# Performance work log

Measured on AMD Instinct MI355X. Metric: run time of the kernel, lower is better.

Reference implementation:

```python
import jax, jax.numpy as jnp
import numpy as np

N_NODES = 50000


def _gat_layer(h, e_feat, Ww, Wb, aw, ab, src, dst):
    # h: [N,1,din], e_feat: [E,1,edim]
    hs = h[src]                                   # [E,1,din] gather src
    hd = h[dst]                                   # [E,1,din] gather dst
    # edge attention logit: relu(attn_fc(cat(src,dst)))
    e = jax.nn.relu(jnp.concatenate([hs, hd], axis=-1) @ aw.T + ab)  # [E,1,1]
    # segment softmax over incoming edges of each dst node
    emax = jax.ops.segment_max(e, dst, num_segments=N_NODES)          # [N,1,1]
    ex = jnp.exp(e - emax[dst])
    denom = jax.ops.segment_sum(ex, dst, num_segments=N_NODES)        # [N,1,1]
    alpha = ex / denom[dst]                                           # [E,1,1]
    # weighted scatter-sum of edge messages (m = edge features)
    z = jax.ops.segment_sum(alpha * e_feat, dst, num_segments=N_NODES)  # [N,1,edim]
    # node update: relu(W_apply(cat(h, z)))
    return jax.nn.relu(jnp.concatenate([h, z], axis=-1) @ Ww.T + Wb)    # [N,1,dout]


def setup_inputs() -> dict:
    key = jax.random.key(0)
    ks = jax.random.split(key, 12)
    N, E, D = N_NODES, 640000, 128
    s = 0.05  # weight scale for numerical sanity
    return {
        "nfeats": jax.random.normal(ks[0], (N, 1, D), jnp.float32),
        "efeats": jax.random.normal(ks[1], (E, 1, D), jnp.float32),
        "W_apply_w0": jax.random.normal(ks[2], (D, 2 * D), jnp.float32) * s,
        "W_apply_b0": jax.random.normal(ks[3], (D,), jnp.float32) * s,
        "attn_w0": jax.random.normal(ks[4], (1, 2 * D), jnp.float32) * s,
        "attn_b0": jax.random.normal(ks[5], (1,), jnp.float32) * s,
        "W_apply_w1": jax.random.normal(ks[6], (D, 2 * D), jnp.float32) * s,
        "W_apply_b1": jax.random.normal(ks[7], (D,), jnp.float32) * s,
        "attn_w1": jax.random.normal(ks[8], (1, 2 * D), jnp.float32) * s,
        "attn_b1": jax.random.normal(ks[9], (1,), jnp.float32) * s,
        "src": jax.random.randint(ks[10], (E,), 0, N, jnp.int32),
        "dst": jax.random.randint(ks[11], (E,), 0, N, jnp.int32),
    }


def reference(nfeats, efeats, W_apply_w0, W_apply_b0, attn_w0, attn_b0,
              W_apply_w1, W_apply_b1, attn_w1, attn_b1, src, dst):
    h = _gat_layer(nfeats, efeats, W_apply_w0, W_apply_b0, attn_w0, attn_b0, src, dst)
    # dropout is identity in eval mode
    h = _gat_layer(h, efeats, W_apply_w1, W_apply_b1, attn_w1, attn_b1, src, dst)
    return h.sum(axis=1)  # [N, dout]
```

## Files before the change

### kernel.cpp

```cpp
#include <hip/hip_runtime.h>


__global__ void hist_k(const int* __restrict__ dst, int* __restrict__ counts, int E){
  int e = blockIdx.x*blockDim.x + threadIdx.x;
  if(e<E) atomicAdd(&counts[dst[e]], 1);
}

__global__ __launch_bounds__(1024) void scan1_k(const int* __restrict__ counts, int* __restrict__ excl,
                                                int* __restrict__ partials, int N){
  __shared__ int tmp[1024];
  int tid = threadIdx.x;
  int i = blockIdx.x*1024 + tid;
  int v = (i<N)? counts[i] : 0;
  tmp[tid] = v;
  __syncthreads();
  for(int off=1; off<1024; off<<=1){
    int t = (tid>=off)? tmp[tid-off] : 0;
    __syncthreads();
    tmp[tid] += t;
    __syncthreads();
  }
  if(i<N) excl[i] = tmp[tid] - v;
  if(tid==1023) partials[blockIdx.x] = tmp[tid];
}

__global__ void scan2_k(int* __restrict__ partials, int NB){
  __shared__ int tmp[64];
  int tid = threadIdx.x;
  int v = (tid<NB)? partials[tid] : 0;
  tmp[tid] = v;
  __syncthreads();
  for(int off=1; off<64; off<<=1){
    int t = (tid>=off)? tmp[tid-off] : 0;
    __syncthreads();
    tmp[tid] += t;
    __syncthreads();
  }
  if(tid<NB) partials[tid] = tmp[tid] - v;
}

__global__ __launch_bounds__(1024) void scan3_k(int* __restrict__ row_ptr, const int* __restrict__ partials,
                                                int* __restrict__ cursors, int N, int E){
  int i = blockIdx.x*1024 + threadIdx.x;
  if(i<N){
    int r = row_ptr[i] + partials[blockIdx.x];
    row_ptr[i] = r;
    cursors[i] = r;
  }
  if(i==0) row_ptr[N] = E;
}

__global__ void scatter_k(const int* __restrict__ src, const int* __restrict__ dst, int* __restrict__ cursors,
                          int2* __restrict__ edat, int E){
  int e = blockIdx.x*blockDim.x + threadIdx.x;
  if(e<E){
    int d = dst[e];
    int p = atomicAdd(&cursors[d], 1);
    edat[p] = make_int2(e, src[e]);
  }
}

__global__ void wt_k(const float* __restrict__ W, float* __restrict__ Wt){
  int idx = blockIdx.x*256 + threadIdx.x;
  int k = idx >> 7, o = idx & 127;
  Wt[idx] = W[o*256 + k];
}


__global__ void attn_k(const float* __restrict__ h, const float* __restrict__ aw, const float* __restrict__ ab,
                       float* __restrict__ a_src, float* __restrict__ a_dst, int N){
  int gid = blockIdx.x*blockDim.x + threadIdx.x;
  int n = gid >> 6, lane = gid & 63;
  if(n >= N) return;
  float2 hv = ((const float2*)(h + (size_t)n*128))[lane];
  float2 wa = ((const float2*)aw)[lane];
  float2 wb = ((const float2*)(aw+128))[lane];
  float s = hv.x*wa.x + hv.y*wa.y;
  float t = hv.x*wb.x + hv.y*wb.y;
  #pragma unroll
  for(int off=32; off>0; off>>=1){
    s += __shfl_xor(s, off, 64);
    t += __shfl_xor(t, off, 64);
  }
  if(lane==0){ a_src[n] = s; a_dst[n] = t + ab[0]; }
}

__global__ __launch_bounds__(256) void agg_k(const float* __restrict__ efeats,
    const float* __restrict__ a_src, const float* __restrict__ a_dst,
    const int* __restrict__ row_ptr, const int2* __restrict__ edat,
    float* __restrict__ z, int N){
  int gid = blockIdx.x*blockDim.x + threadIdx.x;
  int n = gid >> 6, lane = gid & 63;
  if(n >= N) return;
  int half = lane >> 5, l32 = lane & 31;
  int beg = row_ptr[n], end = row_ptr[n+1];
  int deg = end - beg;
  if(deg <= 0){
    if(half==0) ((float4*)z)[(size_t)n*32 + l32] = make_float4(0.f,0.f,0.f,0.f);
    return;
  }
  float adn = a_dst[n];

  int i = beg + lane;
  bool valid = i < end;
  int2 es = valid ? edat[i] : make_int2(0,0);
  int perm_reg = es.x;
  float e_reg = valid ? fmaxf(a_src[es.y] + adn, 0.f) : -1e30f;

  float m = e_reg;
  #pragma unroll
  for(int off=32; off>0; off>>=1) m = fmaxf(m, __shfl_xor(m, off, 64));
  for(int c = beg + 64; c < end; c += 64){
    int ii = c + lane;
    float ev = (ii < end) ? fmaxf(a_src[edat[ii].y] + adn, 0.f) : -1e30f;
    #pragma unroll
    for(int off=32; off>0; off>>=1) ev = fmaxf(ev, __shfl_xor(ev, off, 64));
    m = fmaxf(m, ev);
  }

  float ex_reg = valid ? __expf(e_reg - m) : 0.f;
  float s = ex_reg;
  #pragma unroll
  for(int off=32; off>0; off>>=1) s += __shfl_xor(s, off, 64);
  for(int c = beg + 64; c < end; c += 64){
    int ii = c + lane;
    float ev = (ii < end) ? __expf(fmaxf(a_src[edat[ii].y] + adn, 0.f) - m) : 0.f;
    #pragma unroll
    for(int off=32; off>0; off>>=1) ev += __shfl_xor(ev, off, 64);
    s += ev;
  }
  float inv = 1.f / s;

  const float4* ef4 = (const float4*)efeats;
  float4 acc = make_float4(0.f,0.f,0.f,0.f);
  int cnt = min(deg, 64);
  int j = 0;
  for(; j + 8 <= cnt; j += 8){
    float p0 = __shfl(ex_reg, j+half,   64); int r0 = __shfl(perm_reg, j+half,   64);
    float p1 = __shfl(ex_reg, j+2+half, 64); int r1 = __shfl(perm_reg, j+2+half, 64);
    float p2 = __shfl(ex_reg, j+4+half, 64); int r2 = __shfl(perm_reg, j+4+half, 64);
    float p3 = __shfl(ex_reg, j+6+half, 64); int r3 = __shfl(perm_reg, j+6+half, 64);
    float4 f0 = ef4[(size_t)r0*32 + l32];
    float4 f1 = ef4[(size_t)r1*32 + l32];
    float4 f2 = ef4[(size_t)r2*32 + l32];
    float4 f3 = ef4[(size_t)r3*32 + l32];
    acc.x += p0*f0.x; acc.y += p0*f0.y; acc.z += p0*f0.z; acc.w += p0*f0.w;
    acc.x += p1*f1.x; acc.y += p1*f1.y; acc.z += p1*f1.z; acc.w += p1*f1.w;
    acc.x += p2*f2.x; acc.y += p2*f2.y; acc.z += p2*f2.z; acc.w += p2*f2.w;
    acc.x += p3*f3.x; acc.y += p3*f3.y; acc.z += p3*f3.z; acc.w += p3*f3.w;
  }
  for(; j + 2 <= cnt; j += 2){
    float p = __shfl(ex_reg, j+half, 64); int r = __shfl(perm_reg, j+half, 64);
    float4 f = ef4[(size_t)r*32 + l32];
    acc.x += p*f.x; acc.y += p*f.y; acc.z += p*f.z; acc.w += p*f.w;
  }
  if(j < cnt){
    float p = __shfl(ex_reg, j, 64); int r = __shfl(perm_reg, j, 64);
    if(half==0){
      float4 f = ef4[(size_t)r*32 + l32];
      acc.x += p*f.x; acc.y += p*f.y; acc.z += p*f.z; acc.w += p*f.w;
    }
  }
  for(int c = beg + 64; c < end; c += 64){
    int ii = c + lane;
    bool v2 = ii < end;
    int2 es2 = v2 ? edat[ii] : make_int2(0,0);
    int pr = es2.x;
    float er = v2 ? __expf(fmaxf(a_src[es2.y] + adn, 0.f) - m) : 0.f;
    int cc = min(end - c, 64);
    int jj = 0;
    for(; jj + 2 <= cc; jj += 2){
      float p = __shfl(er, jj+half, 64); int r = __shfl(pr, jj+half, 64);
      float4 f = ef4[(size_t)r*32 + l32];
      acc.x += p*f.x; acc.y += p*f.y; acc.z += p*f.z; acc.w += p*f.w;
    }
    if(jj < cc){
      float p = __shfl(er, jj, 64); int r = __shfl(pr, jj, 64);
      if(half==0){
        float4 f = ef4[(size_t)r*32 + l32];
        acc.x += p*f.x; acc.y += p*f.y; acc.z += p*f.z; acc.w += p*f.w;
      }
    }
  }

  acc.x += __shfl_xor(acc.x, 32, 64);
  acc.y += __shfl_xor(acc.y, 32, 64);
  acc.z += __shfl_xor(acc.z, 32, 64);
  acc.w += __shfl_xor(acc.w, 32, 64);
  if(half==0){
    acc.x *= inv; acc.y *= inv; acc.z *= inv; acc.w *= inv;
    ((float4*)z)[(size_t)n*32 + l32] = acc;
  }
}

__global__ __launch_bounds__(256) void update_k(const float* __restrict__ h, const float* __restrict__ z,
                                                const float* __restrict__ Wt, const float* __restrict__ bias,
                                                float* __restrict__ out, int N){
  __shared__ float xsT[32][132];
  __shared__ float ws[32][132];
  int tid = threadIdx.x;
  int tx = tid & 15;
  int ty = tid >> 4;
  int n0 = blockIdx.x * 128;

  int sn  = tid >> 1;
  int skc = (tid & 1) * 16;
  int wkk = tid >> 3;
  int woc = (tid & 7) * 4;

  float4 xv4[4], wv4[4];
  {
    int node = n0 + sn;
    bool v = node < N;
    const float* sp = h + (size_t)node*128 + skc;
    #pragma unroll
    for(int jj=0;jj<4;jj++) xv4[jj] = v ? ((const float4*)sp)[jj] : make_float4(0.f,0.f,0.f,0.f);
    const float* wp = Wt + (size_t)wkk*128 + woc;
    #pragma unroll
    for(int jj=0;jj<4;jj++) wv4[jj] = *(const float4*)(wp + jj*32);
  }

  float acc[8][8];
  #pragma unroll
  for(int i=0;i<8;i++)
    #pragma unroll
    for(int j2=0;j2<8;j2++) acc[i][j2] = 0.f;

  for(int kb=0; kb<256; kb+=32){
    #pragma unroll
    for(int jj=0;jj<4;jj++){
      int kq = skc + jj*4;
      xsT[kq+0][sn] = xv4[jj].x;
      xsT[kq+1][sn] = xv4[jj].y;
      xsT[kq+2][sn] = xv4[jj].z;
      xsT[kq+3][sn] = xv4[jj].w;
      *(float4*)&ws[wkk][woc + jj*32] = wv4[jj];
    }
    __syncthreads();

    if(kb + 32 < 256){
      int kb2 = kb + 32;
      int node = n0 + sn;
      bool v = node < N;
      const float* sp = (kb2 < 128) ? h + (size_t)node*128 + kb2 + skc
                                    : z + (size_t)node*128 + (kb2-128) + skc;
      #pragma unroll
      for(int jj=0;jj<4;jj++) xv4[jj] = v ? ((const float4*)sp)[jj] : make_float4(0.f,0.f,0.f,0.f);
      const float* wp = Wt + (size_t)(kb2 + wkk)*128 + woc;
      #pragma unroll
      for(int jj=0;jj<4;jj++) wv4[jj] = *(const float4*)(wp + jj*32);
    }

    #pragma unroll 8
    for(int k=0;k<32;k++){
      float4 x0 = *(const float4*)&xsT[k][ty*4];
      float4 x1 = *(const float4*)&xsT[k][64 + ty*4];
      float4 w0 = *(const float4*)&ws[k][tx*4];
      float4 w1 = *(const float4*)&ws[k][64 + tx*4];
      float xv[8] = {x0.x,x0.y,x0.z,x0.w, x1.x,x1.y,x1.z,x1.w};
      float wv[8] = {w0.x,w0.y,w0.z,w0.w, w1.x,w1.y,w1.z,w1.w};
      #pragma unroll
      for(int i=0;i<8;i++)
        #pragma unroll
        for(int j2=0;j2<8;j2++)
          acc[i][j2] += xv[i]*wv[j2];
    }
    __syncthreads();
  }

  const float4* b4 = (const float4*)bias;
  float4 bb0 = b4[tx];
  float4 bb1 = b4[16 + tx];
  #pragma unroll
  for(int i=0;i<8;i++){
    int n = n0 + ((i<4) ? (ty*4 + i) : (64 + ty*4 + (i-4)));
    if(n >= N) continue;
    float4 r0, r1;
    r0.x = fmaxf(acc[i][0]+bb0.x, 0.f);
    r0.y = fmaxf(acc[i][1]+bb0.y, 0.f);
    r0.z = fmaxf(acc[i][2]+bb0.z, 0.f);
    r0.w = fmaxf(acc[i][3]+bb0.w, 0.f);
    r1.x = fmaxf(acc[i][4]+bb1.x, 0.f);
    r1.y = fmaxf(acc[i][5]+bb1.y, 0.f);
    r1.z = fmaxf(acc[i][6]+bb1.z, 0.f);
    r1.w = fmaxf(acc[i][7]+bb1.w, 0.f);
    *(float4*)(out + (size_t)n*128 + tx*4)      = r0;
    *(float4*)(out + (size_t)n*128 + 64 + tx*4) = r1;
  }
}


extern "C" void kernel_launch(void* const* d_in, const int* in_sizes, int n_in,
                              void* d_out, int out_size, void* d_ws, size_t ws_size,
                              hipStream_t stream){
  const float* nfeats = (const float*)d_in[0];
  const float* efeats = (const float*)d_in[1];
  const float* Ww0 = (const float*)d_in[2];
  const float* Wb0 = (const float*)d_in[3];
  const float* aw0 = (const float*)d_in[4];
  const float* ab0 = (const float*)d_in[5];
  const float* Ww1 = (const float*)d_in[6];
  const float* Wb1 = (const float*)d_in[7];
  const float* aw1 = (const float*)d_in[8];
  const float* ab1 = (const float*)d_in[9];
  const int* src = (const int*)d_in[10];
  const int* dst = (const int*)d_in[11];
  int E = in_sizes[10];
  int N = in_sizes[0] / 128;

  char* base = (char*)d_ws;
  size_t off = 0;
  auto take = [&](size_t bytes) -> char* {
    char* p = base + off;
    off = (off + bytes + 255) & ~(size_t)255;
    return p;
  };
  int*   counts  = (int*)take((size_t)N*4);
  int*   row_ptr = (int*)take((size_t)(N+1)*4);
  int*   cursors = (int*)take((size_t)N*4);
  int*   partials= (int*)take(256);
  int2*  edat    = (int2*)take((size_t)E*8);
  float* a_src   = (float*)take((size_t)N*4);
  float* a_dst   = (float*)take((size_t)N*4);
  float* zbuf    = (float*)take((size_t)N*128*4);
  float* h1      = (float*)take((size_t)N*128*4);
  float* Wt0     = (float*)take((size_t)256*128*4);
  float* Wt1     = (float*)take((size_t)256*128*4);

  int NB = (N + 1023)/1024;

  hipMemsetAsync(counts, 0, (size_t)N*4, stream);
  wt_k<<<128, 256, 0, stream>>>(Ww0, Wt0);
  wt_k<<<128, 256, 0, stream>>>(Ww1, Wt1);
  hist_k<<<(E+255)/256, 256, 0, stream>>>(dst, counts, E);
  scan1_k<<<NB, 1024, 0, stream>>>(counts, row_ptr, partials, N);
  scan2_k<<<1, 64, 0, stream>>>(partials, NB);
  scan3_k<<<NB, 1024, 0, stream>>>(row_ptr, partials, cursors, N, E);
  scatter_k<<<(E+255)/256, 256, 0, stream>>>(src, dst, cursors, edat, E);

  int agrid = (N + 3)/4;
  int ugrid = (N + 127)/128;
  attn_k<<<agrid, 256, 0, stream>>>(nfeats, aw0, ab0, a_src, a_dst, N);
  agg_k<<<agrid, 256, 0, stream>>>(efeats, a_src, a_dst, row_ptr, edat, zbuf, N);
  update_k<<<ugrid, 256, 0, stream>>>(nfeats, zbuf, Wt0, Wb0, h1, N);
  attn_k<<<agrid, 256, 0, stream>>>(h1, aw1, ab1, a_src, a_dst, N);
  agg_k<<<agrid, 256, 0, stream>>>(efeats, a_src, a_dst, row_ptr, edat, zbuf, N);
  update_k<<<ugrid, 256, 0, stream>>>(h1, zbuf, Wt1, Wb1, (float*)d_out, N);
}
```

Measured before the change: 773.8 us.

## Fuse CSR preprocessing kernels, single-block scan, and shrink update tile to 64 nodes

Merges the two weight transposes and the dst histogram into one grid-stride kernel. It replaces the three-kernel block scan with a single 1024-thread block that does a wave-shuffle scan with a running carry. It also fuses the edge scatter into the first attention-logit kernel. Separately, the node update GEMM now uses 64-node tiles with 128 threads, doubling the block count for better CU coverage. The goal is to cut kernel launches and serialization, at the cost of a serial single-block scan and less per-block reuse of the weight tiles.

```diff
diff --git a/kernel.cpp b/kernel.cpp
--- a/kernel.cpp
+++ b/kernel.cpp
@@ -1,71 +1,85 @@
 #include <hip/hip_runtime.h>
 
-
-__global__ void hist_k(const int* __restrict__ dst, int* __restrict__ counts, int E){
-  int e = blockIdx.x*blockDim.x + threadIdx.x;
-  if(e<E) atomicAdd(&counts[dst[e]], 1);
-}
-
-__global__ __launch_bounds__(1024) void scan1_k(const int* __restrict__ counts, int* __restrict__ excl,
-                                                int* __restrict__ partials, int N){
-  __shared__ int tmp[1024];
+__global__ void prep_k(const float* __restrict__ Ww0, const float* __restrict__ Ww1,
+                       float* __restrict__ Wt0, float* __restrict__ Wt1,
+                       const int* __restrict__ dst, int* __restrict__ counts, int E){
+  int gid = blockIdx.x*blockDim.x + threadIdx.x;
+  int gstride = gridDim.x*blockDim.x;
+  for(int idx = gid; idx < 2*32768; idx += gstride){
+    int w = idx >> 15, r = idx & 32767;
+    int k = r >> 7, o = r & 127;
+    float v = (w==0 ? Ww0 : Ww1)[o*256 + k];
+    (w==0 ? Wt0 : Wt1)[r] = v;
+  }
+  for(int e = gid; e < E; e += gstride) atomicAdd(&counts[dst[e]], 1);
+}
+
+__global__ __launch_bounds__(1024) void scan_k(const int* __restrict__ counts,
+                                               int* __restrict__ row_ptr, int* __restrict__ cursors,
+                                               int N, int E){
+  __shared__ int wsum[16];
+  __shared__ int carry;
   int tid = threadIdx.x;
-  int i = blockIdx.x*1024 + tid;
-  int v = (i<N)? counts[i] : 0;
-  tmp[tid] = v;
+  int lane = tid & 63, wv = tid >> 6;
+  if(tid==0) carry = 0;
   __syncthreads();
-  for(int off=1; off<1024; off<<=1){
-    int t = (tid>=off)? tmp[tid-off] : 0;
-    __syncthreads();
-    tmp[tid] += t;
-    __syncthreads();
-  }
-  if(i<N) excl[i] = tmp[tid] - v;
-  if(tid==1023) partials[blockIdx.x] = tmp[tid];
-}
-
-__global__ void scan2_k(int* __restrict__ partials, int NB){
-  __shared__ int tmp[64];
-  int tid = threadIdx.x;
-  int v = (tid<NB)? partials[tid] : 0;
-  tmp[tid] = v;
-  __syncthreads();
-  for(int off=1; off<64; off<<=1){
-    int t = (tid>=off)? tmp[tid-off] : 0;
-    __syncthreads();
-    tmp[tid] += t;
-    __syncthreads();
-  }
-  if(tid<NB) partials[tid] = tmp[tid] - v;
-}
-
-__global__ __launch_bounds__(1024) void scan3_k(int* __restrict__ row_ptr, const int* __restrict__ partials,
-                                                int* __restrict__ cursors, int N, int E){
-  int i = blockIdx.x*1024 + threadIdx.x;
-  if(i<N){
-    int r = row_ptr[i] + partials[blockIdx.x];
-    row_ptr[i] = r;
-    cursors[i] = r;
-  }
-  if(i==0) row_ptr[N] = E;
-}
-
-__global__ void scatter_k(const int* __restrict__ src, const int* __restrict__ dst, int* __restrict__ cursors,
-                          int2* __restrict__ edat, int E){
-  int e = blockIdx.x*blockDim.x + threadIdx.x;
-  if(e<E){
-    int d = dst[e];
+  for(int base = 0; base < N; base += 1024){
+    int i = base + tid;
+    int v = (i<N) ? counts[i] : 0;
+    int x = v;
+    #pragma unroll
+    for(int off=1; off<64; off<<=1){
+      int t = __shfl_up(x, off, 64);
+      if(lane >= off) x += t;
+    }
+    if(lane==63) wsum[wv] = x;
+    __syncthreads();
+    if(tid < 16){
+      int w = wsum[tid];
+      #pragma unroll
+      for(int off=1; off<16; off<<=1){
+        int t = __shfl_up(w, off, 64);
+        if(tid >= off) w += t;
+      }
+      wsum[tid] = w;
+    }
+    __syncthreads();
+    int prev = (wv==0) ? 0 : wsum[wv-1];
+    int ex = carry + prev + x - v;
+    if(i<N){ row_ptr[i] = ex; cursors[i] = ex; }
+    __syncthreads();
+    if(tid==0) carry += wsum[15];
+    __syncthreads();
+  }
+  if(tid==0) row_ptr[N] = E;
+}
+
+__global__ void scat_attn_k(const int* __restrict__ src, const int* __restrict__ dst,
+                            int* __restrict__ cursors, int2* __restrict__ edat, int E,
+                            const float* __restrict__ h, const float* __restrict__ aw,
+                            const float* __restrict__ ab,
+                            float* __restrict__ a_src, float* __restrict__ a_dst, int N){
+  int gid = blockIdx.x*blockDim.x + threadIdx.x;
+  if(gid < E){
+    int d = dst[gid];
     int p = atomicAdd(&cursors[d], 1);
-    edat[p] = make_int2(e, src[e]);
-  }
-}
-
-__global__ void wt_k(const float* __restrict__ W, float* __restrict__ Wt){
-  int idx = blockIdx.x*256 + threadIdx.x;
-  int k = idx >> 7, o = idx & 127;
-  Wt[idx] = W[o*256 + k];
-}
-
+    edat[p] = make_int2(gid, src[gid]);
+  }
+  int n = gid >> 6, lane = gid & 63;
+  if(n < N){
+    float2 hv = ((const float2*)(h + (size_t)n*128))[lane];
+    float2 wa = ((const float2*)aw)[lane];
+    float2 wb = ((const float2*)(aw+128))[lane];
+    float s = hv.x*wa.x + hv.y*wa.y;
+    float t = hv.x*wb.x + hv.y*wb.y;
+    #pragma unroll
+    for(int off=32; off>0; off>>=1){
+      s += __shfl_xor(s, off, 64);
+      t += __shfl_xor(t, off, 64);
+    }
+    if(lane==0){ a_src[n] = s; a_dst[n] = t + ab[0]; }
+  }
+}
 
 __global__ void attn_k(const float* __restrict__ h, const float* __restrict__ aw, const float* __restrict__ ab,
                        float* __restrict__ a_src, float* __restrict__ a_dst, int N){
@@ -193,31 +207,29 @@
   }
 }
 
-__global__ __launch_bounds__(256) void update_k(const float* __restrict__ h, const float* __restrict__ z,
+__global__ __launch_bounds__(128) void update_k(const float* __restrict__ h, const float* __restrict__ z,
                                                 const float* __restrict__ Wt, const float* __restrict__ bias,
                                                 float* __restrict__ out, int N){
-  __shared__ float xsT[32][132];
+  __shared__ float xsT[32][68];
   __shared__ float ws[32][132];
   int tid = threadIdx.x;
   int tx = tid & 15;
   int ty = tid >> 4;
-  int n0 = blockIdx.x * 128;
+  int n0 = blockIdx.x * 64;
 
   int sn  = tid >> 1;
   int skc = (tid & 1) * 16;
-  int wkk = tid >> 3;
-  int woc = (tid & 7) * 4;
-
-  float4 xv4[4], wv4[4];
+
+  float4 xv4[4], wv4[8];
   {
     int node = n0 + sn;
     bool v = node < N;
     const float* sp = h + (size_t)node*128 + skc;
     #pragma unroll
     for(int jj=0;jj<4;jj++) xv4[jj] = v ? ((const float4*)sp)[jj] : make_float4(0.f,0.f,0.f,0.f);
-    const float* wp = Wt + (size_t)wkk*128 + woc;
-    #pragma unroll
-    for(int jj=0;jj<4;jj++) wv4[jj] = *(const float4*)(wp + jj*32);
+    const float4* wp = (const float4*)Wt;
+    #pragma unroll
+    for(int jj=0;jj<8;jj++) wv4[jj] = wp[jj*128 + tid];
   }
 
   float acc[8][8];
@@ -234,7 +246,13 @@
       xsT[kq+1][sn] = xv4[jj].y;
       xsT[kq+2][sn] = xv4[jj].z;
       xsT[kq+3][sn] = xv4[jj].w;
-      *(float4*)&ws[wkk][woc + jj*32] = wv4[jj];
+    }
+    #pragma unroll
+    for(int jj=0;jj<8;jj++){
+      int fidx = jj*128 + tid;
+      int k = fidx >> 5;
+      int c = (fidx & 31) << 2;
+      *(float4*)&ws[k][c] = wv4[jj];
     }
     __syncthreads();
 
@@ -246,15 +264,15 @@
                                     : z + (size_t)node*128 + (kb2-128) + skc;
       #pragma unroll
       for(int jj=0;jj<4;jj++) xv4[jj] = v ? ((const float4*)sp)[jj] : make_float4(0.f,0.f,0.f,0.f);
-      const float* wp = Wt + (size_t)(kb2 + wkk)*128 + woc;
+      const float4* wp = (const float4*)(Wt + (size_t)kb2*128);
       #pragma unroll
-      for(int jj=0;jj<4;jj++) wv4[jj] = *(const float4*)(wp + jj*32);
+      for(int jj=0;jj<8;jj++) wv4[jj] = wp[jj*128 + tid];
     }
 
     #pragma unroll 8
     for(int k=0;k<32;k++){
       float4 x0 = *(const float4*)&xsT[k][ty*4];
-      float4 x1 = *(const float4*)&xsT[k][64 + ty*4];
+      float4 x1 = *(const float4*)&xsT[k][32 + ty*4];
       float4 w0 = *(const float4*)&ws[k][tx*4];
       float4 w1 = *(const float4*)&ws[k][64 + tx*4];
       float xv[8] = {x0.x,x0.y,x0.z,x0.w, x1.x,x1.y,x1.z,x1.w};
@@ -273,7 +291,7 @@
   float4 bb1 = b4[16 + tx];
   #pragma unroll
   for(int i=0;i<8;i++){
-    int n = n0 + ((i<4) ? (ty*4 + i) : (64 + ty*4 + (i-4)));
+    int n = n0 + ((i<4) ? (ty*4 + i) : (32 + ty*4 + (i-4)));
     if(n >= N) continue;
     float4 r0, r1;
     r0.x = fmaxf(acc[i][0]+bb0.x, 0.f);
@@ -318,7 +336,6 @@
   int*   counts  = (int*)take((size_t)N*4);
   int*   row_ptr = (int*)take((size_t)(N+1)*4);
   int*   cursors = (int*)take((size_t)N*4);
-  int*   partials= (int*)take(256);
   int2*  edat    = (int2*)take((size_t)E*8);
   float* a_src   = (float*)take((size_t)N*4);
   float* a_dst   = (float*)take((size_t)N*4);
@@ -327,23 +344,17 @@
   float* Wt0     = (float*)take((size_t)256*128*4);
   float* Wt1     = (float*)take((size_t)256*128*4);
 
-  int NB = (N + 1023)/1024;
-
   hipMemsetAsync(counts, 0, (size_t)N*4, stream);
-  wt_k<<<128, 256, 0, stream>>>(Ww0, Wt0);
-  wt_k<<<128, 256, 0, stream>>>(Ww1, Wt1);
-  hist_k<<<(E+255)/256, 256, 0, stream>>>(dst, counts, E);
-  scan1_k<<<NB, 1024, 0, stream>>>(counts, row_ptr, partials, N);
-  scan2_k<<<1, 64, 0, stream>>>(partials, NB);
-  scan3_k<<<NB, 1024, 0, stream>>>(row_ptr, partials, cursors, N, E);
-  scatter_k<<<(E+255)/256, 256, 0, stream>>>(src, dst, cursors, edat, E);
+  prep_k<<<2500, 256, 0, stream>>>(Ww0, Ww1, Wt0, Wt1, dst, counts, E);
+  scan_k<<<1, 1024, 0, stream>>>(counts, row_ptr, cursors, N, E);
 
   int agrid = (N + 3)/4;
-  int ugrid = (N + 127)/128;
-  attn_k<<<agrid, 256, 0, stream>>>(nfeats, aw0, ab0, a_src, a_dst, N);
+  int ugrid = (N + 63)/64;
+  scat_attn_k<<<agrid, 256, 0, stream>>>(src, dst, cursors, edat, E,
+                                         nfeats, aw0, ab0, a_src, a_dst, N);
   agg_k<<<agrid, 256, 0, stream>>>(efeats, a_src, a_dst, row_ptr, edat, zbuf, N);
-  update_k<<<ugrid, 256, 0, stream>>>(nfeats, zbuf, Wt0, Wb0, h1, N);
+  update_k<<<ugrid, 128, 0, stream>>>(nfeats, zbuf, Wt0, Wb0, h1, N);
   attn_k<<<agrid, 256, 0, stream>>>(h1, aw1, ab1, a_src, a_dst, N);
   agg_k<<<agrid, 256, 0, stream>>>(efeats, a_src, a_dst, row_ptr, edat, zbuf, N);
-  update_k<<<ugrid, 256, 0, stream>>>(h1, zbuf, Wt1, Wb1, (float*)d_out, N);
-}
+  update_k<<<ugrid, 128, 0, stream>>>(h1, zbuf, Wt1, Wb1, (float*)d_out, N);
+}
```

Result: slower. 845.4 us (+9.3%).
